# Kernel tuning notes

Measured on AMD Instinct MI355X. Metric: run time of the kernel, lower is better.

The kernel has to match this reference:

```python
import jax, jax.numpy as jnp
import numpy as np

# Model dims (GatedAttentionLayer of Qwen3.5 ANE hybrid stack)
C = 2048      # hidden_size
H = 16        # num_attention_heads
HK = 4        # num_key_value_heads
D = 128       # head_dim
ROT = 32      # rotary_dim = head_dim * partial_rotary_factor (0.25)
S = 1024      # sequence length (prefill)
CTX = 1024    # kv cache context length
N_ATTN = 6    # number of full-attention layers -> kv_cache leading dim 2*N_ATTN
EPS = 1e-6
ROPE_THETA = 1e7


def _rotate_half(x):
    h = x.shape[-1] // 2
    return jnp.concatenate([-x[..., h:], x[..., :h]], axis=-1)


def _rms_norm(x, w, eps=EPS):
    # Qwen3.5 convention: stored weight is (w - 1), applied as (1 + weight)
    r = jax.lax.rsqrt(jnp.mean(x * x, axis=-1, keepdims=True) + eps)
    return x * r * (1.0 + w)


def setup_inputs() -> dict:
    key = jax.random.key(0)
    ks = jax.random.split(key, 6)
    hidden_states = jax.random.normal(ks[0], (1, C, 1, S), jnp.float32)
    q_proj_w = jax.random.normal(ks[1], (H * 2 * D, C), jnp.float32) * 0.02  # q + gate
    k_proj_w = jax.random.normal(ks[2], (HK * D, C), jnp.float32) * 0.02
    v_proj_w = jax.random.normal(ks[3], (HK * D, C), jnp.float32) * 0.02
    o_proj_w = jax.random.normal(ks[4], (C, H * D), jnp.float32) * 0.02
    q_norm_w = jnp.zeros((D,), jnp.float32)
    k_norm_w = jnp.zeros((D,), jnp.float32)
    kv_cache = jnp.zeros((2 * N_ATTN, HK, CTX, D), jnp.float32)
    position_ids = jnp.arange(S, dtype=jnp.int32)
    # causal mask: 0 on/below diagonal, -1e9 above
    causal_mask = jnp.where(
        jnp.arange(CTX)[None, :] <= jnp.arange(S)[:, None], 0.0, -1e9
    ).astype(jnp.float32)[None, None]  # [1,1,S,CTX]
    # RoPE tables over rotary_dim
    inv_freq = 1.0 / (ROPE_THETA ** (jnp.arange(0, ROT, 2, dtype=jnp.float32) / ROT))
    t = jnp.arange(CTX, dtype=jnp.float32)
    freqs = jnp.outer(t, inv_freq)          # [CTX, ROT//2]
    emb = jnp.concatenate([freqs, freqs], -1)  # [CTX, ROT]
    cos_cached = jnp.cos(emb)
    sin_cached = jnp.sin(emb)
    return dict(hidden_states=hidden_states, q_proj_w=q_proj_w, k_proj_w=k_proj_w,
                v_proj_w=v_proj_w, o_proj_w=o_proj_w, q_norm_w=q_norm_w,
                k_norm_w=k_norm_w, kv_cache=kv_cache, causal_mask=causal_mask,
                position_ids=position_ids, cos_cached=cos_cached,
                sin_cached=sin_cached, attn_layer_idx=0)


def reference(hidden_states, q_proj_w, k_proj_w, v_proj_w, o_proj_w,
              q_norm_w, k_norm_w, kv_cache, causal_mask, position_ids,
              cos_cached, sin_cached, attn_layer_idx):
    x = hidden_states[0, :, 0, :]                     # [C, S]
    q_raw = q_proj_w @ x                              # [H*2D, S]  (1x1 Conv2d == GEMM)
    qg = q_raw.reshape(H, 2 * D, S)
    q = jnp.transpose(qg[:, :D, :], (0, 2, 1))        # [H, S, D]
    gate = jnp.transpose(qg[:, D:, :], (0, 2, 1))     # [H, S, D]
    k = jnp.transpose((k_proj_w @ x).reshape(HK, D, S), (0, 2, 1))  # [HK, S, D]
    v = jnp.transpose((v_proj_w @ x).reshape(HK, D, S), (0, 2, 1))  # [HK, S, D]

    q = _rms_norm(q, q_norm_w)
    k = _rms_norm(k, k_norm_w)

    cos = cos_cached[position_ids]   # [S, ROT]
    sin = sin_cached[position_ids]

    def rope(t):
        rot, pas = t[..., :ROT], t[..., ROT:]
        rot = rot * cos + _rotate_half(rot) * sin
        return jnp.concatenate([rot, pas], axis=-1)

    q, k = rope(q), rope(k)

    # prefill cache write at pos_start = position_ids[0]
    k_idx = 2 * attn_layer_idx
    v_idx = k_idx + 1
    pos_start = position_ids[0]
    kv_cache = jax.lax.dynamic_update_slice(kv_cache, k[None], (k_idx, 0, pos_start, 0))
    kv_cache = jax.lax.dynamic_update_slice(kv_cache, v[None], (v_idx, 0, pos_start, 0))

    g = H // HK  # GQA repeat (expand+reshape == contiguous repeat)
    k_full = jnp.repeat(kv_cache[k_idx], g, axis=0)   # [H, CTX, D]
    v_full = jnp.repeat(kv_cache[v_idx], g, axis=0)   # [H, CTX, D]

    scale = D ** -0.5
    attn = jnp.einsum('hsd,htd->hst', q, k_full) * scale + causal_mask[0]
    attn = jax.nn.softmax(attn, axis=-1)
    out = jnp.einsum('hst,htd->hsd', attn, v_full)    # [H, S, D]
    out = out * jax.nn.sigmoid(gate)
    out = jnp.transpose(out, (0, 2, 1)).reshape(H * D, S)
    output = (o_proj_w @ out)[None, :, None, :]       # [1, C, 1, S]
    return output
```

## Files before the change

### kernel.cpp

```cpp
#include <hip/hip_runtime.h>
#include <cstdint>

#define S_LEN 1024
#define C_DIM 2048
#define NH    16
#define NHK   4
#define HD    128
#define ROT   32
#define SCALE 0.08838834764831845f

typedef __bf16 bf16x8 __attribute__((ext_vector_type(8)));
typedef float floatx4 __attribute__((ext_vector_type(4)));
typedef float floatx16 __attribute__((ext_vector_type(16)));
typedef unsigned short ushortx8 __attribute__((ext_vector_type(8)));

__device__ __forceinline__ unsigned short f2bf(float f) {
  union { float f; uint32_t u; } x; x.f = f;
  uint32_t r = (x.u + 0x7fffu + ((x.u >> 16) & 1u)) >> 16;
  return (unsigned short)r;
}
__device__ __forceinline__ float bf2f(unsigned short v) {
  union { uint32_t u; float f; } x; x.u = (uint32_t)v << 16; return x.f;
}

__device__ __forceinline__ void async_copy16(const unsigned short* g, unsigned short* l) {
  __builtin_amdgcn_global_load_lds(
      (const __attribute__((address_space(1))) void*)g,
      (__attribute__((address_space(3))) void*)l,
      16, 0, 0);
}

#define WAIT_VM(N) asm volatile("s_waitcnt vmcnt(" #N ")" ::: "memory")

__device__ __forceinline__ void bar_lds_only() {
  asm volatile("s_waitcnt lgkmcnt(0)" ::: "memory");
  __builtin_amdgcn_s_barrier();
}

__device__ __forceinline__ int swz8(int row) { return (row ^ (row >> 3)) & 7; }

__global__ __launch_bounds__(256)
void prep_kernel(const float* __restrict__ qw, const float* __restrict__ kw,
                 const float* __restrict__ vw, const float* __restrict__ ow,
                 unsigned short* __restrict__ wout,
                 const float* __restrict__ x, unsigned short* __restrict__ xT) {
  __shared__ float t[32][33];
  int bid = blockIdx.x;
  if (bid < 14336) {
    const int NQ = 4096 * 2048 / 4, NK = 512 * 2048 / 4, NV = 512 * 2048 / 4;
    int i = bid * 256 + threadIdx.x;
    const float* src; int j;
    if (i < NQ) { src = qw; j = i; }
    else if (i < NQ + NK) { src = kw; j = i - NQ; }
    else if (i < NQ + NK + NV) { src = vw; j = i - NQ - NK; }
    else { src = ow; j = i - NQ - NK - NV; }
    float4 v = ((const float4*)src)[j];
    ushort4 o;
    o.x = f2bf(v.x); o.y = f2bf(v.y); o.z = f2bf(v.z); o.w = f2bf(v.w);
    ((ushort4*)wout)[i] = o;
  } else {
    int b2 = bid - 14336;
    int st = b2 & 31, ct = b2 >> 5;
    int c = threadIdx.x & 31, rq = threadIdx.x >> 5;
#pragma unroll
    for (int i = 0; i < 4; ++i) {
      int r = rq + i * 8;
      t[r][c] = x[(size_t)(ct * 32 + r) * S_LEN + st * 32 + c];
    }
    __syncthreads();
#pragma unroll
    for (int i = 0; i < 4; ++i) {
      int r = rq + i * 8;
      xT[(size_t)(st * 32 + r) * C_DIM + ct * 32 + c] = f2bf(t[c][r]);
    }
  }
}

__device__ __forceinline__ void norm_rope_epi512(
    floatx16& acc, float (*pp)[32],
    const float* __restrict__ w, const int* __restrict__ pos_ids,
    const float* __restrict__ cosc, const float* __restrict__ sinc,
    unsigned short* __restrict__ outp,
    int wave, int lane, int wm, int scol0) {
  int l31 = lane & 31, half = lane >> 5;
  float s = 0.f;
#pragma unroll
  for (int reg = 0; reg < 16; ++reg) { float v = acc[reg]; s += v * v; }
  s += __shfl_xor(s, 32);
  if (half == 0) pp[wave][l31] = s;
  __syncthreads();
  int gb = wave & 4;
  float tot = pp[gb][l31] + pp[gb + 1][l31] + pp[gb + 2][l31] + pp[gb + 3][l31];
  float rn = rsqrtf(tot * (1.0f / 128.0f) + 1e-6f);
  int scol = scol0 + l31;
  int pos = pos_ids[scol];
  bool rope = (wm == 0);
#pragma unroll
  for (int g = 0; g < 4; ++g) {
    int dbase = wm + half * 4 + g * 8;
    ushort4 o;
#pragma unroll
    for (int rr = 0; rr < 4; ++rr) {
      int reg = g * 4 + rr;
      int d = dbase + rr;
      float v = acc[reg] * rn * (1.0f + w[d]);
      if (rope) {
        float cv = cosc[pos * ROT + d], sv = sinc[pos * ROT + d];
        int d2 = (d < 16) ? d + 16 : d - 16;
        float pv = acc[reg ^ 8] * rn * (1.0f + w[d2]);
        v = v * cv + ((d < 16) ? -pv : pv) * sv;
      }
      ((unsigned short*)&o)[rr] = f2bf(v);
    }
    *(ushort4*)&outp[(size_t)scol * HD + dbase] = o;
  }
}

#define GEMM512_CORE(EXTRA_LB)                                                     \
  int tid = threadIdx.x, wave = tid >> 6, lane = tid & 63;                         \
  int l31 = lane & 31, half = lane >> 5;                                           \
  int wm = (wave & 3) * 32, wn = (wave >> 2) * 32;                                 \
  int m0 = blockIdx.x * 128, n0 = blockIdx.y * 64;                                 \
  int r8 = tid >> 3, c8 = tid & 7;                                                 \
  int arow1 = r8 + 64;                                                             \
  int apos0 = c8 ^ swz8(r8), apos1 = c8 ^ swz8(arow1), bpos = apos0;               \
  int aswz = swz8(wm + l31), bswz = swz8(wn + l31);                                \
  const unsigned short* Ag = A + (size_t)m0 * C_DIM;                               \
  const unsigned short* Bg = BT + (size_t)n0 * C_DIM;                              \
  floatx16 acc = (floatx16)0.f;                                                    \
  ushortx8 rA0, rA1, rB;                                                           \
  rA0 = *(const ushortx8*)(Ag + (size_t)r8 * C_DIM + c8 * 8);                      \
  rA1 = *(const ushortx8*)(Ag + (size_t)arow1 * C_DIM + c8 * 8);                   \
  rB  = *(const ushortx8*)(Bg + (size_t)r8 * C_DIM + c8 * 8);                      \
  *(ushortx8*)&Asm[0][r8 * 64 + apos0 * 8] = rA0;                                  \
  *(ushortx8*)&Asm[0][arow1 * 64 + apos1 * 8] = rA1;                               \
  *(ushortx8*)&Bsm[0][r8 * 64 + bpos * 8] = rB;                                    \
  bar_lds_only();                                                                  \
  for (int t = 0; t < 32; ++t) {                                                   \
    int b = t & 1;                                                                 \
    if (t < 31) {                                                                  \
      int kt = (t + 1) * 64;                                                       \
      rA0 = *(const ushortx8*)(Ag + (size_t)r8 * C_DIM + kt + c8 * 8);             \
      rA1 = *(const ushortx8*)(Ag + (size_t)arow1 * C_DIM + kt + c8 * 8);          \
      rB  = *(const ushortx8*)(Bg + (size_t)r8 * C_DIM + kt + c8 * 8);             \
    }                                                                              \
    _Pragma("unroll")                                                              \
    for (int kb = 0; kb < 4; ++kb) {                                               \
      int ca = (((kb << 1) | half) ^ aswz) << 3;                                   \
      int cb = (((kb << 1) | half) ^ bswz) << 3;                                   \
      bf16x8 av = *(const bf16x8*)&Asm[b][(wm + l31) * 64 + ca];                   \
      bf16x8 bv = *(const bf16x8*)&Bsm[b][(wn + l31) * 64 + cb];                   \
      acc = __builtin_amdgcn_mfma_f32_32x32x16_bf16(av, bv, acc, 0, 0, 0);         \
    }                                                                              \
    if (t < 31) {                                                                  \
      *(ushortx8*)&Asm[b ^ 1][r8 * 64 + apos0 * 8] = rA0;                          \
      *(ushortx8*)&Asm[b ^ 1][arow1 * 64 + apos1 * 8] = rA1;                       \
      *(ushortx8*)&Bsm[b ^ 1][r8 * 64 + bpos * 8] = rB;                            \
    }                                                                              \
    bar_lds_only();                                                                \
  }

__global__ __launch_bounds__(512, 6)
void gemm_qkv_fused(const unsigned short* __restrict__ A,
                    const unsigned short* __restrict__ BT,
                    const float* __restrict__ qw, const float* __restrict__ kw,
                    const int* __restrict__ pos_ids,
                    const float* __restrict__ cosc, const float* __restrict__ sinc,
                    unsigned short* __restrict__ qb, unsigned short* __restrict__ kbuf,
                    unsigned short* __restrict__ vTb, unsigned short* __restrict__ sgb) {
  __shared__ unsigned short Asm[2][128 * 64];
  __shared__ unsigned short Bsm[2][64 * 64];
  __shared__ float pp[8][32];
  GEMM512_CORE()

  int scol0 = n0 + wn;
  int ty = blockIdx.x;
  if (ty < 32) {
    int h = ty >> 1;
    if ((ty & 1) == 0) {
      norm_rope_epi512(acc, pp, qw, pos_ids, cosc, sinc,
                       qb + (size_t)h * S_LEN * HD, wave, lane, wm, scol0);
    } else {
      int scol = scol0 + l31;
#pragma unroll
      for (int g = 0; g < 4; ++g) {
        int dbase = wm + half * 4 + g * 8;
        ushort4 o;
#pragma unroll
        for (int rr = 0; rr < 4; ++rr)
          ((unsigned short*)&o)[rr] = f2bf(1.0f / (1.0f + __expf(-acc[g * 4 + rr])));
        *(ushort4*)&sgb[((size_t)h * S_LEN + scol) * HD + dbase] = o;
      }
    }
  } else if (ty < 36) {
    int hk = ty - 32;
    norm_rope_epi512(acc, pp, kw, pos_ids, cosc, sinc,
                     kbuf + (size_t)hk * S_LEN * HD, wave, lane, wm, scol0);
  } else {
    int hk = ty - 36;
#pragma unroll
    for (int reg = 0; reg < 16; ++reg) {
      int d = wm + (reg & 3) + 8 * (reg >> 2) + 4 * half;
      vTb[(size_t)hk * HD * S_LEN + (size_t)d * S_LEN + scol0 + l31] = f2bf(acc[reg]);
    }
  }
}

__global__ __launch_bounds__(512, 6)
void gemm_oproj(const unsigned short* __restrict__ A,
                const unsigned short* __restrict__ BT,
                float* __restrict__ C) {
  __shared__ unsigned short Asm[2][128 * 64];
  __shared__ unsigned short Bsm[2][64 * 64];
  GEMM512_CORE()

#pragma unroll
  for (int reg = 0; reg < 16; ++reg) {
    int row = m0 + wm + (reg & 3) + 8 * (reg >> 2) + 4 * half;
    C[(size_t)row * S_LEN + n0 + wn + l31] = acc[reg];
  }
}

__global__ __launch_bounds__(256)
void attn_kernel(const unsigned short* __restrict__ qb,
                 const unsigned short* __restrict__ kbuf,
                 const unsigned short* __restrict__ vTb,
                 const unsigned short* __restrict__ sgb,
                 unsigned short* __restrict__ outT) {
  __shared__ __align__(16) unsigned short Ks[2][64 * 128];
  __shared__ __align__(16) unsigned short Vs[128 * 64];
  __shared__ __align__(16) unsigned short Ps[4][16][72];
  int h = blockIdx.x, qt = blockIdx.y;
  int s0 = qt * 64;
  int hk = h >> 2;
  int tid = threadIdx.x, wave = tid >> 6, lane = tid & 63;
  int l16 = lane & 15, quad = lane >> 4;
  int lsw = l16 & 7;

  const unsigned short* qg = qb + ((size_t)(h * S_LEN + s0 + wave * 16 + l16)) * HD;
  bf16x8 qfr[4];
#pragma unroll
  for (int kb = 0; kb < 4; ++kb)
    qfr[kb] = *(const bf16x8*)(qg + kb * 32 + quad * 8);
  asm volatile("" :: "v"(qfr[0]), "v"(qfr[1]), "v"(qfr[2]), "v"(qfr[3]));
  WAIT_VM(0);

  float m_r[4], l_r[4];
#pragma unroll
  for (int r = 0; r < 4; ++r) { m_r[r] = -1e30f; l_r[r] = 0.f; }
  floatx4 acc_o[8];
#pragma unroll
  for (int i = 0; i < 8; ++i) acc_o[i] = (floatx4)0.f;
  int srow_base = s0 + wave * 16 + quad * 4;

  const unsigned short* kg0 = kbuf + (size_t)hk * S_LEN * HD;
  const unsigned short* vg0 = vTb + (size_t)hk * HD * S_LEN;

  int kr4 = lane >> 4, kc16 = lane & 15;
  int vr8 = lane >> 3, vc8 = lane & 7;

#define STAGE_K(BUF, T)                                                    \
  { _Pragma("unroll")                                                      \
    for (int i = 0; i < 4; ++i) {                                          \
      int rbase = wave * 16 + i * 4;                                       \
      int row = rbase + kr4;                                               \
      int cs = kc16 ^ (row & 7);                                           \
      async_copy16(kg0 + (size_t)((T) * 64 + row) * HD + cs * 8,           \
                   &Ks[BUF][rbase * 128]); } }
#define STAGE_V(T)                                                         \
  { _Pragma("unroll")                                                      \
    for (int i = 0; i < 4; ++i) {                                          \
      int rbase = wave * 32 + i * 8;                                       \
      int row = rbase + vr8;                                               \
      int cs = vc8 ^ (row & 7);                                            \
      async_copy16(vg0 + (size_t)row * S_LEN + (T) * 64 + cs * 8,          \
                   Vs + rbase * 64); } }

  STAGE_K(0, 0)
  STAGE_V(0)

  for (int t = 0; t <= qt; ++t) {
    int cur = t & 1;
    bool more = (t < qt);
    if (more) { STAGE_K(cur ^ 1, t + 1) WAIT_VM(8); }
    else      { WAIT_VM(4); }
    __builtin_amdgcn_s_barrier();

    floatx4 acc_s[4];
#pragma unroll
    for (int ni = 0; ni < 4; ++ni) acc_s[ni] = (floatx4)0.f;
#pragma unroll
    for (int kb = 0; kb < 4; ++kb) {
#pragma unroll
      for (int ni = 0; ni < 4; ++ni) {
        int cl = (kb * 4 + quad) ^ lsw;
        bf16x8 bk = *(const bf16x8*)&Ks[cur][(ni * 16 + l16) * 128 + cl * 8];
        acc_s[ni] = __builtin_amdgcn_mfma_f32_16x16x32_bf16(qfr[kb], bk, acc_s[ni], 0, 0, 0);
      }
    }

    int jt = t * 64;
    bool diag = (t == qt);
    float alpha[4];
#pragma unroll
    for (int r = 0; r < 4; ++r) {
      float scv[4];
      float mx = -1e30f;
#pragma unroll
      for (int ni = 0; ni < 4; ++ni) {
        float sv = acc_s[ni][r] * SCALE;
        if (diag) {
          int jg = jt + ni * 16 + l16;
          if (jg > srow_base + r) sv = -1e30f;
        }
        scv[ni] = sv;
        mx = fmaxf(mx, sv);
      }
#pragma unroll
      for (int off = 8; off; off >>= 1) mx = fmaxf(mx, __shfl_xor(mx, off, 16));
      float mnew = fmaxf(m_r[r], mx);
      float psv = 0.f;
#pragma unroll
      for (int ni = 0; ni < 4; ++ni) {
        float pv = (scv[ni] > -1e29f) ? __expf(scv[ni] - mnew) : 0.f;
        Ps[wave][quad * 4 + r][ni * 16 + l16] = f2bf(pv);
        psv += pv;
      }
#pragma unroll
      for (int off = 8; off; off >>= 1) psv += __shfl_xor(psv, off, 16);
      alpha[r] = __expf(m_r[r] - mnew);
      m_r[r] = mnew;
      l_r[r] = l_r[r] * alpha[r] + psv;
    }
#pragma unroll
    for (int i = 0; i < 8; ++i)
#pragma unroll
      for (int r = 0; r < 4; ++r) acc_o[i][r] *= alpha[r];

    if (more) { WAIT_VM(4); }
    else      { WAIT_VM(0); }
    __builtin_amdgcn_s_barrier();

#pragma unroll
    for (int kb2 = 0; kb2 < 2; ++kb2) {
      bf16x8 ap = *(const bf16x8*)&Ps[wave][l16][kb2 * 32 + quad * 8];
#pragma unroll
      for (int ni2 = 0; ni2 < 8; ++ni2) {
        int cl = (kb2 * 4 + quad) ^ lsw;
        bf16x8 bv = *(const bf16x8*)&Vs[(ni2 * 16 + l16) * 64 + cl * 8];
        acc_o[ni2] = __builtin_amdgcn_mfma_f32_16x16x32_bf16(ap, bv, acc_o[ni2], 0, 0, 0);
      }
    }
    __builtin_amdgcn_s_barrier();
    if (more) { STAGE_V(t + 1) }
  }

#pragma unroll
  for (int r = 0; r < 4; ++r) {
    int s = srow_base + r;
    float inv = 1.0f / l_r[r];
    const unsigned short* sgp = sgb + ((size_t)h * S_LEN + s) * HD;
    unsigned short* op = outT + (size_t)s * (NH * HD) + h * HD;
#pragma unroll
    for (int ni2 = 0; ni2 < 8; ++ni2) {
      int d = ni2 * 16 + l16;
      op[d] = f2bf(acc_o[ni2][r] * inv * bf2f(sgp[d]));
    }
  }
#undef STAGE_K
#undef STAGE_V
}

extern "C" void kernel_launch(void* const* d_in, const int* in_sizes, int n_in,
                              void* d_out, int out_size, void* d_ws, size_t ws_size,
                              hipStream_t stream) {
  const float* hs       = (const float*)d_in[0];
  const float* q_proj_w = (const float*)d_in[1];
  const float* k_proj_w = (const float*)d_in[2];
  const float* v_proj_w = (const float*)d_in[3];
  const float* o_proj_w = (const float*)d_in[4];
  const float* q_norm_w = (const float*)d_in[5];
  const float* k_norm_w = (const float*)d_in[6];
  const int*   pos_ids  = (const int*)d_in[9];
  const float* cos_c    = (const float*)d_in[10];
  const float* sin_c    = (const float*)d_in[11];
  float* out = (float*)d_out;

  char* ws = (char*)d_ws;
  unsigned short* wqkv = (unsigned short*)(ws + 0);
  unsigned short* wo   = (unsigned short*)(ws + 20971520);
  unsigned short* xT   = (unsigned short*)(ws + 29360128);
  unsigned short* qb   = (unsigned short*)(ws + 33554432);
  unsigned short* kbuf = (unsigned short*)(ws + 37748736);
  unsigned short* vTb  = (unsigned short*)(ws + 38797312);
  unsigned short* sgb  = (unsigned short*)(ws + 39845888);
  unsigned short* aoT  = (unsigned short*)(ws + 44040192);

  prep_kernel<<<14336 + 2048, 256, 0, stream>>>(q_proj_w, k_proj_w, v_proj_w, o_proj_w,
                                                wqkv, hs, xT);
  gemm_qkv_fused<<<dim3(40, 16), 512, 0, stream>>>(wqkv, xT, q_norm_w, k_norm_w,
                                                   pos_ids, cos_c, sin_c,
                                                   qb, kbuf, vTb, sgb);
  attn_kernel<<<dim3(16, 16), 256, 0, stream>>>(qb, kbuf, vTb, sgb, aoT);
  gemm_oproj<<<dim3(16, 16), 512, 0, stream>>>(wo, aoT, out);
}
```

Measured before the change: 240.6 us.

## Split attention into single-wave blocks that each stage their own K/V tiles

The attention kernel now launches one 64-thread block per 16-row query slice, with a third grid dimension, instead of four waves sharing one 64-row tile. Each wave stages the full K and V tiles into its own LDS and uses only waitcnt ordering, so every s_barrier is removed. The cost is four times as many K/V loads into LDS. Because each block still holds about 49KB of LDS for a single wave, far fewer waves fit on a CU, which may hide latency less well.

Result: slower. 248.0 us (+3.0%).

```diff
diff --git a/kernel.cpp b/kernel.cpp
--- a/kernel.cpp
+++ b/kernel.cpp
@@ -31,6 +31,7 @@
 }
 
 #define WAIT_VM(N) asm volatile("s_waitcnt vmcnt(" #N ")" ::: "memory")
+#define WAIT_LGKM0 asm volatile("s_waitcnt lgkmcnt(0)" ::: "memory")
 
 __device__ __forceinline__ void bar_lds_only() {
   asm volatile("s_waitcnt lgkmcnt(0)" ::: "memory");
@@ -221,7 +222,7 @@
   }
 }
 
-__global__ __launch_bounds__(256)
+__global__ __launch_bounds__(64)
 void attn_kernel(const unsigned short* __restrict__ qb,
                  const unsigned short* __restrict__ kbuf,
                  const unsigned short* __restrict__ vTb,
@@ -229,15 +230,15 @@
                  unsigned short* __restrict__ outT) {
   __shared__ __align__(16) unsigned short Ks[2][64 * 128];
   __shared__ __align__(16) unsigned short Vs[128 * 64];
-  __shared__ __align__(16) unsigned short Ps[4][16][72];
-  int h = blockIdx.x, qt = blockIdx.y;
+  __shared__ __align__(16) unsigned short Ps[16][72];
+  int h = blockIdx.x, qt = blockIdx.y, qq = blockIdx.z;
   int s0 = qt * 64;
   int hk = h >> 2;
-  int tid = threadIdx.x, wave = tid >> 6, lane = tid & 63;
+  int lane = threadIdx.x & 63;
   int l16 = lane & 15, quad = lane >> 4;
   int lsw = l16 & 7;
 
-  const unsigned short* qg = qb + ((size_t)(h * S_LEN + s0 + wave * 16 + l16)) * HD;
+  const unsigned short* qg = qb + ((size_t)(h * S_LEN + s0 + qq * 16 + l16)) * HD;
   bf16x8 qfr[4];
 #pragma unroll
   for (int kb = 0; kb < 4; ++kb)
@@ -251,7 +252,7 @@
   floatx4 acc_o[8];
 #pragma unroll
   for (int i = 0; i < 8; ++i) acc_o[i] = (floatx4)0.f;
-  int srow_base = s0 + wave * 16 + quad * 4;
+  int srow_base = s0 + qq * 16 + quad * 4;
 
   const unsigned short* kg0 = kbuf + (size_t)hk * S_LEN * HD;
   const unsigned short* vg0 = vTb + (size_t)hk * HD * S_LEN;
@@ -261,16 +262,16 @@
 
 #define STAGE_K(BUF, T)                                                    \
   { _Pragma("unroll")                                                      \
-    for (int i = 0; i < 4; ++i) {                                          \
-      int rbase = wave * 16 + i * 4;                                       \
+    for (int i = 0; i < 16; ++i) {                                         \
+      int rbase = i * 4;                                                   \
       int row = rbase + kr4;                                               \
       int cs = kc16 ^ (row & 7);                                           \
       async_copy16(kg0 + (size_t)((T) * 64 + row) * HD + cs * 8,           \
                    &Ks[BUF][rbase * 128]); } }
 #define STAGE_V(T)                                                         \
   { _Pragma("unroll")                                                      \
-    for (int i = 0; i < 4; ++i) {                                          \
-      int rbase = wave * 32 + i * 8;                                       \
+    for (int i = 0; i < 16; ++i) {                                         \
+      int rbase = i * 8;                                                   \
       int row = rbase + vr8;                                               \
       int cs = vc8 ^ (row & 7);                                            \
       async_copy16(vg0 + (size_t)row * S_LEN + (T) * 64 + cs * 8,          \
@@ -282,9 +283,9 @@
   for (int t = 0; t <= qt; ++t) {
     int cur = t & 1;
     bool more = (t < qt);
-    if (more) { STAGE_K(cur ^ 1, t + 1) WAIT_VM(8); }
-    else      { WAIT_VM(4); }
-    __builtin_amdgcn_s_barrier();
+    WAIT_LGKM0;
+    if (more) { STAGE_K(cur ^ 1, t + 1) WAIT_VM(16); }
+    else      { WAIT_VM(0); }
 
     floatx4 acc_s[4];
 #pragma unroll
@@ -323,7 +324,7 @@
 #pragma unroll
       for (int ni = 0; ni < 4; ++ni) {
         float pv = (scv[ni] > -1e29f) ? __expf(scv[ni] - mnew) : 0.f;
-        Ps[wave][quad * 4 + r][ni * 16 + l16] = f2bf(pv);
+        Ps[quad * 4 + r][ni * 16 + l16] = f2bf(pv);
         psv += pv;
       }
 #pragma unroll
@@ -337,13 +338,9 @@
 #pragma unroll
       for (int r = 0; r < 4; ++r) acc_o[i][r] *= alpha[r];
 
-    if (more) { WAIT_VM(4); }
-    else      { WAIT_VM(0); }
-    __builtin_amdgcn_s_barrier();
-
 #pragma unroll
     for (int kb2 = 0; kb2 < 2; ++kb2) {
-      bf16x8 ap = *(const bf16x8*)&Ps[wave][l16][kb2 * 32 + quad * 8];
+      bf16x8 ap = *(const bf16x8*)&Ps[l16][kb2 * 32 + quad * 8];
 #pragma unroll
       for (int ni2 = 0; ni2 < 8; ++ni2) {
         int cl = (kb2 * 4 + quad) ^ lsw;
@@ -351,8 +348,10 @@
         acc_o[ni2] = __builtin_amdgcn_mfma_f32_16x16x32_bf16(ap, bv, acc_o[ni2], 0, 0, 0);
       }
     }
-    __builtin_amdgcn_s_barrier();
-    if (more) { STAGE_V(t + 1) }
+    if (more) {
+      WAIT_LGKM0;
+      STAGE_V(t + 1)
+    }
   }
 
 #pragma unroll
@@ -401,6 +400,6 @@
   gemm_qkv_fused<<<dim3(40, 16), 512, 0, stream>>>(wqkv, xT, q_norm_w, k_norm_w,
                                                    pos_ids, cos_c, sin_c,
                                                    qb, kbuf, vTb, sgb);
-  attn_kernel<<<dim3(16, 16), 256, 0, stream>>>(qb, kbuf, vTb, sgb, aoT);
+  attn_kernel<<<dim3(16, 16, 4), 64, 0, stream>>>(qb, kbuf, vTb, sgb, aoT);
   gemm_oproj<<<dim3(16, 16), 512, 0, stream>>>(wo, aoT, out);
 }
```
